# Performance work log

Measured on AMD Instinct MI355X. Metric: run time of the kernel, lower is better.

Reference implementation:

```python
import jax, jax.numpy as jnp
import numpy as np

N = 100000
DEG = 16
E = N * DEG
IN_F = 128
OUT_F = 64
ALPHA = 0.2  # LeakyReLU negative slope


def setup_inputs() -> dict:
    key = jax.random.key(0)
    k1, k2, k3, k4, k5, k6 = jax.random.split(key, 6)
    x = jax.random.normal(k1, (N, IN_F), dtype=jnp.float32)
    # src = repeat(arange(N), DEG) guarantees every node has outgoing edges
    # (original torch code divides by the out-edge score sum -> NaN otherwise).
    src = jnp.repeat(jnp.arange(N, dtype=jnp.int64), DEG)
    dst = jax.random.randint(k2, (E,), 0, N, dtype=jnp.int64)
    edges = jnp.stack([src, dst], axis=0)
    # Conv1d(in, out, k=1, bias=False) == linear with weight [out, in]
    w_seq = jax.random.normal(k3, (OUT_F, IN_F), dtype=jnp.float32) / np.sqrt(IN_F)
    # a_1, a_2: Conv1d(out, 1, k=1) with bias
    a1_w = jax.random.normal(k4, (OUT_F,), dtype=jnp.float32) / np.sqrt(OUT_F)
    a1_b = jnp.zeros((), dtype=jnp.float32)
    a2_w = jax.random.normal(k5, (OUT_F,), dtype=jnp.float32) / np.sqrt(OUT_F)
    a2_b = jnp.zeros((), dtype=jnp.float32)
    bias = jnp.zeros((OUT_F,), dtype=jnp.float32)
    return {"x": x, "edges": edges, "w_seq": w_seq, "a1_w": a1_w,
            "a1_b": a1_b, "a2_w": a2_w, "a2_b": a2_b, "bias": bias}


def reference(x, edges, w_seq, a1_w, a1_b, a2_w, a2_b, bias):
    src, dst = edges[0], edges[1]
    feat = x @ w_seq.T                       # [N, OUT_F]
    a1 = feat @ a1_w + a1_b                  # [N]
    a2 = feat @ a2_w + a2_b                  # [N]
    score = a1[src] + a2[dst]                # [E]
    score = jnp.exp(jax.nn.leaky_relu(score, ALPHA))
    score_sum = jax.ops.segment_sum(score, src, num_segments=N)  # [N]
    # sparse COO (score at (src,dst)) @ feat == segment_sum of score * feat[dst]
    msgs = score[:, None] * feat[dst]        # [E, OUT_F]
    agg = jax.ops.segment_sum(msgs, src, num_segments=N)         # [N, OUT_F]
    out = agg / score_sum[:, None] + bias
    return out
```

## Files before the change

kernel.cpp:

```cpp
#include <hip/hip_runtime.h>
#include <stdint.h>

#define N_NODES 100000
#define DEG 16
#define IN_F 128
#define OUT_F 64
#define ALPHA 0.2f

typedef __attribute__((ext_vector_type(8))) short short8;
typedef __attribute__((ext_vector_type(4))) float f32x4;
typedef __attribute__((ext_vector_type(4))) int i32x4;
typedef __attribute__((ext_vector_type(2))) unsigned int u32x2;

static __device__ __forceinline__ short f2bf(float f) {
    uint32_t u = __float_as_uint(f);
    u += 0x7FFFu + ((u >> 16) & 1u);
    return (short)(u >> 16);
}

__global__ __launch_bounds__(256) void w_conv_kernel(const float* __restrict__ w,
                                                     unsigned short* __restrict__ wb) {
    int idx = blockIdx.x * 256 + threadIdx.x;
    if (idx < OUT_F * IN_F) wb[idx] = (unsigned short)f2bf(w[idx]);
}

__global__ __launch_bounds__(256) void gat_feat_kernel(
    const float* __restrict__ x, const unsigned short* __restrict__ wb,
    const float* __restrict__ a1w, const float* __restrict__ a1bp,
    const float* __restrict__ a2w, const float* __restrict__ a2bp,
    unsigned short* __restrict__ featb, float* __restrict__ a1,
    float* __restrict__ a2)
{
    __shared__ __align__(16) unsigned short lds[4][32][64];
    const int wid  = threadIdx.x >> 6;
    const int lane = threadIdx.x & 63;
    const int r = lane & 15;
    const int g = lane >> 4;
    const int base = (blockIdx.x * 4 + wid) * 32;
    if (base >= N_NODES) return;

    short8 bfrag[4][4];
    #pragma unroll
    for (int ft = 0; ft < 4; ++ft)
        #pragma unroll
        for (int ks = 0; ks < 4; ++ks)
            bfrag[ft][ks] = *(const short8*)(wb + (ft * 16 + r) * IN_F + ks * 32 + g * 8);

    f32x4 acc[2][4];
    #pragma unroll
    for (int mt = 0; mt < 2; ++mt)
        #pragma unroll
        for (int ft = 0; ft < 4; ++ft) acc[mt][ft] = (f32x4){0.f, 0.f, 0.f, 0.f};

    #pragma unroll
    for (int mt = 0; mt < 2; ++mt) {
        const float* xrow = x + (size_t)(base + mt * 16 + r) * IN_F;
        #pragma unroll
        for (int ks = 0; ks < 4; ++ks) {
            const float* xp = xrow + ks * 32 + g * 8;
            f32x4 x0 = *(const f32x4*)(xp);
            f32x4 x1 = *(const f32x4*)(xp + 4);
            short8 af;
            af[0] = f2bf(x0[0]); af[1] = f2bf(x0[1]);
            af[2] = f2bf(x0[2]); af[3] = f2bf(x0[3]);
            af[4] = f2bf(x1[0]); af[5] = f2bf(x1[1]);
            af[6] = f2bf(x1[2]); af[7] = f2bf(x1[3]);
            #pragma unroll
            for (int ft = 0; ft < 4; ++ft)
                acc[mt][ft] = __builtin_amdgcn_mfma_f32_16x16x32_bf16(af, bfrag[ft][ks], acc[mt][ft], 0, 0, 0);
        }
    }

    float w1v[4], w2v[4];
    #pragma unroll
    for (int ft = 0; ft < 4; ++ft) { w1v[ft] = a1w[ft * 16 + r]; w2v[ft] = a2w[ft * 16 + r]; }
    float p1[2][4] = {{0.f,0.f,0.f,0.f},{0.f,0.f,0.f,0.f}};
    float p2[2][4] = {{0.f,0.f,0.f,0.f},{0.f,0.f,0.f,0.f}};
    #pragma unroll
    for (int mt = 0; mt < 2; ++mt)
        #pragma unroll
        for (int ft = 0; ft < 4; ++ft)
            #pragma unroll
            for (int reg = 0; reg < 4; ++reg) {
                p1[mt][reg] += acc[mt][ft][reg] * w1v[ft];
                p2[mt][reg] += acc[mt][ft][reg] * w2v[ft];
            }
    #pragma unroll
    for (int m = 1; m <= 8; m <<= 1)
        #pragma unroll
        for (int mt = 0; mt < 2; ++mt)
            #pragma unroll
            for (int reg = 0; reg < 4; ++reg) {
                p1[mt][reg] += __shfl_xor(p1[mt][reg], m, 64);
                p2[mt][reg] += __shfl_xor(p2[mt][reg], m, 64);
            }
    if (r == 0) {
        float b1 = a1bp[0], b2 = a2bp[0];
        #pragma unroll
        for (int mt = 0; mt < 2; ++mt)
            #pragma unroll
            for (int reg = 0; reg < 4; ++reg) {
                a1[base + mt * 16 + g * 4 + reg] = p1[mt][reg] + b1;
                a2[base + mt * 16 + g * 4 + reg] = p2[mt][reg] + b2;
            }
    }

    #pragma unroll
    for (int mt = 0; mt < 2; ++mt)
        #pragma unroll
        for (int ft = 0; ft < 4; ++ft)
            #pragma unroll
            for (int reg = 0; reg < 4; ++reg)
                lds[wid][mt * 16 + g * 4 + reg][ft * 16 + r] = (unsigned short)f2bf(acc[mt][ft][reg]);
    const char* lsrc = (const char*)(&lds[wid][0][0]);
    char* gdst = (char*)featb + (size_t)base * (OUT_F * 2);
    #pragma unroll
    for (int t = 0; t < 4; ++t) {
        i32x4 v = *(const i32x4*)(lsrc + t * 1024 + lane * 16);
        *(i32x4*)(gdst + t * 1024 + lane * 16) = v;
    }
}

__global__ __launch_bounds__(256) void gat_agg_kernel(
    const int* __restrict__ dst, const unsigned short* __restrict__ featb,
    const float* __restrict__ a1, const float* __restrict__ a2,
    const float* __restrict__ bias, float* __restrict__ out)
{
    const int wid  = threadIdx.x >> 6;
    const int lane = threadIdx.x & 63;
    const int q  = lane >> 4;
    const int e0 = lane & 15;
    const int i = (blockIdx.x * 4 + wid) * 4 + q;

    const int d = dst[i * DEG + e0];
    const float z = a1[i] + a2[d];
    const float s = __expf(z >= 0.f ? z : ALPHA * z);
    float ssum = s;
    #pragma unroll
    for (int m = 1; m <= 8; m <<= 1) ssum += __shfl_xor(ssum, m, 64);
    const float inv = 1.0f / ssum;

    float acc0 = 0.f, acc1 = 0.f, acc2 = 0.f, acc3 = 0.f;
    const int srcbase = lane & 48;
    #pragma unroll
    for (int e = 0; e < DEG; ++e) {
        const int   de = __shfl(d, srcbase + e, 64);
        const float se = __shfl(s, srcbase + e, 64);
        u32x2 u = *(const u32x2*)(featb + (size_t)(de * OUT_F + e0 * 4));
        acc0 += se * __uint_as_float(u[0] << 16);
        acc1 += se * __uint_as_float(u[0] & 0xffff0000u);
        acc2 += se * __uint_as_float(u[1] << 16);
        acc3 += se * __uint_as_float(u[1] & 0xffff0000u);
    }
    const f32x4 bv = *(const f32x4*)(bias + e0 * 4);
    f32x4 o;
    o[0] = acc0 * inv + bv[0];
    o[1] = acc1 * inv + bv[1];
    o[2] = acc2 * inv + bv[2];
    o[3] = acc3 * inv + bv[3];
    *(f32x4*)(out + (size_t)i * OUT_F + e0 * 4) = o;
}

extern "C" void kernel_launch(void* const* d_in, const int* in_sizes, int n_in,
                              void* d_out, int out_size, void* d_ws, size_t ws_size,
                              hipStream_t stream) {
    (void)in_sizes; (void)n_in; (void)out_size; (void)ws_size;
    const float* x    = (const float*)d_in[0];
    const int*   edges= (const int*)d_in[1];
    const float* w    = (const float*)d_in[2];
    const float* a1w  = (const float*)d_in[3];
    const float* a1b  = (const float*)d_in[4];
    const float* a2w  = (const float*)d_in[5];
    const float* a2b  = (const float*)d_in[6];
    const float* bias = (const float*)d_in[7];
    float* out = (float*)d_out;

    unsigned short* featb = (unsigned short*)d_ws;
    float* a1 = (float*)((char*)d_ws + (size_t)N_NODES * OUT_F * 2);
    float* a2 = a1 + N_NODES;
    unsigned short* wb = (unsigned short*)d_out;

    const int* dst = edges + (size_t)N_NODES * DEG;

    w_conv_kernel<<<dim3((OUT_F * IN_F + 255) / 256), dim3(256), 0, stream>>>(w, wb);
    gat_feat_kernel<<<dim3((N_NODES + 127) / 128), dim3(256), 0, stream>>>(
        x, wb, a1w, a1b, a2w, a2b, featb, a1, a2);
    gat_agg_kernel<<<dim3((N_NODES + 15) / 16), dim3(256), 0, stream>>>(
        dst, featb, a1, a2, bias, out);
}
```

Measured before the change: 58.10 us.

## Fold attention vectors into weights and batch gathers in aggregation

Precomputes v1 = W^T a1w and v2 = W^T a2w in the prep kernel, so a1/a2 are computed as fp32 dot products of x with these vectors during the feature pass. This replaces the post-MFMA projection and its 16-lane shuffle reduction. The aggregation kernel now issues its 16 neighbor gathers in two batches of 8 independent loads to raise memory-level parallelism, with the score shuffles hoisted. The bf16 weight fragments are now loaded per k-step instead of all up front, which lowers register pressure but adds extra loads, and the workspace layout gains v1/v2 and moves wb off the output buffer.

```diff
diff --git a/kernel.cpp b/kernel.cpp
--- a/kernel.cpp
+++ b/kernel.cpp
@@ -12,22 +12,34 @@
 typedef __attribute__((ext_vector_type(4))) int i32x4;
 typedef __attribute__((ext_vector_type(2))) unsigned int u32x2;
 
-static __device__ __forceinline__ short f2bf(float f) {
+static __device__ __forceinline__ unsigned short f2bf(float f) {
     uint32_t u = __float_as_uint(f);
     u += 0x7FFFu + ((u >> 16) & 1u);
-    return (short)(u >> 16);
-}
-
-__global__ __launch_bounds__(256) void w_conv_kernel(const float* __restrict__ w,
-                                                     unsigned short* __restrict__ wb) {
+    return (unsigned short)(u >> 16);
+}
+
+__global__ __launch_bounds__(256) void prep_kernel(
+    const float* __restrict__ w, const float* __restrict__ a1w,
+    const float* __restrict__ a2w, unsigned short* __restrict__ wb,
+    float* __restrict__ v1, float* __restrict__ v2)
+{
     int idx = blockIdx.x * 256 + threadIdx.x;
-    if (idx < OUT_F * IN_F) wb[idx] = (unsigned short)f2bf(w[idx]);
+    if (idx < OUT_F * IN_F) wb[idx] = f2bf(w[idx]);
+    if (blockIdx.x == 0) {
+        int t = threadIdx.x;
+        int k = t & (IN_F - 1);
+        const float* aw = (t < IN_F) ? a1w : a2w;
+        float acc = 0.f;
+        #pragma unroll
+        for (int f = 0; f < OUT_F; ++f) acc += w[f * IN_F + k] * aw[f];
+        if (t < IN_F) v1[k] = acc; else v2[k] = acc;
+    }
 }
 
 __global__ __launch_bounds__(256) void gat_feat_kernel(
     const float* __restrict__ x, const unsigned short* __restrict__ wb,
-    const float* __restrict__ a1w, const float* __restrict__ a1bp,
-    const float* __restrict__ a2w, const float* __restrict__ a2bp,
+    const float* __restrict__ v1, const float* __restrict__ v2,
+    const float* __restrict__ a1bp, const float* __restrict__ a2bp,
     unsigned short* __restrict__ featb, float* __restrict__ a1,
     float* __restrict__ a2)
 {
@@ -39,70 +51,58 @@
     const int base = (blockIdx.x * 4 + wid) * 32;
     if (base >= N_NODES) return;
 
-    short8 bfrag[4][4];
-    #pragma unroll
-    for (int ft = 0; ft < 4; ++ft)
-        #pragma unroll
-        for (int ks = 0; ks < 4; ++ks)
-            bfrag[ft][ks] = *(const short8*)(wb + (ft * 16 + r) * IN_F + ks * 32 + g * 8);
-
     f32x4 acc[2][4];
     #pragma unroll
     for (int mt = 0; mt < 2; ++mt)
         #pragma unroll
         for (int ft = 0; ft < 4; ++ft) acc[mt][ft] = (f32x4){0.f, 0.f, 0.f, 0.f};
-
-    #pragma unroll
-    for (int mt = 0; mt < 2; ++mt) {
-        const float* xrow = x + (size_t)(base + mt * 16 + r) * IN_F;
-        #pragma unroll
-        for (int ks = 0; ks < 4; ++ks) {
-            const float* xp = xrow + ks * 32 + g * 8;
+    float p1[2] = {0.f, 0.f}, p2[2] = {0.f, 0.f};
+
+    #pragma unroll
+    for (int ks = 0; ks < 4; ++ks) {
+        short8 bf[4];
+        #pragma unroll
+        for (int ft = 0; ft < 4; ++ft)
+            bf[ft] = *(const short8*)(wb + (ft * 16 + r) * IN_F + ks * 32 + g * 8);
+        const float* vp1 = v1 + ks * 32 + g * 8;
+        const float* vp2 = v2 + ks * 32 + g * 8;
+        f32x4 v10 = *(const f32x4*)(vp1),     v11 = *(const f32x4*)(vp1 + 4);
+        f32x4 v20 = *(const f32x4*)(vp2),     v21 = *(const f32x4*)(vp2 + 4);
+        #pragma unroll
+        for (int mt = 0; mt < 2; ++mt) {
+            const float* xp = x + (size_t)(base + mt * 16 + r) * IN_F + ks * 32 + g * 8;
             f32x4 x0 = *(const f32x4*)(xp);
             f32x4 x1 = *(const f32x4*)(xp + 4);
+            #pragma unroll
+            for (int j = 0; j < 4; ++j) {
+                p1[mt] += x0[j] * v10[j] + x1[j] * v11[j];
+                p2[mt] += x0[j] * v20[j] + x1[j] * v21[j];
+            }
             short8 af;
-            af[0] = f2bf(x0[0]); af[1] = f2bf(x0[1]);
-            af[2] = f2bf(x0[2]); af[3] = f2bf(x0[3]);
-            af[4] = f2bf(x1[0]); af[5] = f2bf(x1[1]);
-            af[6] = f2bf(x1[2]); af[7] = f2bf(x1[3]);
+            af[0] = (short)f2bf(x0[0]); af[1] = (short)f2bf(x0[1]);
+            af[2] = (short)f2bf(x0[2]); af[3] = (short)f2bf(x0[3]);
+            af[4] = (short)f2bf(x1[0]); af[5] = (short)f2bf(x1[1]);
+            af[6] = (short)f2bf(x1[2]); af[7] = (short)f2bf(x1[3]);
             #pragma unroll
             for (int ft = 0; ft < 4; ++ft)
-                acc[mt][ft] = __builtin_amdgcn_mfma_f32_16x16x32_bf16(af, bfrag[ft][ks], acc[mt][ft], 0, 0, 0);
+                acc[mt][ft] = __builtin_amdgcn_mfma_f32_16x16x32_bf16(af, bf[ft], acc[mt][ft], 0, 0, 0);
         }
     }
 
-    float w1v[4], w2v[4];
-    #pragma unroll
-    for (int ft = 0; ft < 4; ++ft) { w1v[ft] = a1w[ft * 16 + r]; w2v[ft] = a2w[ft * 16 + r]; }
-    float p1[2][4] = {{0.f,0.f,0.f,0.f},{0.f,0.f,0.f,0.f}};
-    float p2[2][4] = {{0.f,0.f,0.f,0.f},{0.f,0.f,0.f,0.f}};
-    #pragma unroll
-    for (int mt = 0; mt < 2; ++mt)
-        #pragma unroll
-        for (int ft = 0; ft < 4; ++ft)
-            #pragma unroll
-            for (int reg = 0; reg < 4; ++reg) {
-                p1[mt][reg] += acc[mt][ft][reg] * w1v[ft];
-                p2[mt][reg] += acc[mt][ft][reg] * w2v[ft];
-            }
-    #pragma unroll
-    for (int m = 1; m <= 8; m <<= 1)
-        #pragma unroll
-        for (int mt = 0; mt < 2; ++mt)
-            #pragma unroll
-            for (int reg = 0; reg < 4; ++reg) {
-                p1[mt][reg] += __shfl_xor(p1[mt][reg], m, 64);
-                p2[mt][reg] += __shfl_xor(p2[mt][reg], m, 64);
-            }
-    if (r == 0) {
+    #pragma unroll
+    for (int mt = 0; mt < 2; ++mt) {
+        p1[mt] += __shfl_xor(p1[mt], 16, 64);
+        p1[mt] += __shfl_xor(p1[mt], 32, 64);
+        p2[mt] += __shfl_xor(p2[mt], 16, 64);
+        p2[mt] += __shfl_xor(p2[mt], 32, 64);
+    }
+    if (lane < 16) {
         float b1 = a1bp[0], b2 = a2bp[0];
         #pragma unroll
-        for (int mt = 0; mt < 2; ++mt)
-            #pragma unroll
-            for (int reg = 0; reg < 4; ++reg) {
-                a1[base + mt * 16 + g * 4 + reg] = p1[mt][reg] + b1;
-                a2[base + mt * 16 + g * 4 + reg] = p2[mt][reg] + b2;
-            }
+        for (int mt = 0; mt < 2; ++mt) {
+            a1[base + mt * 16 + lane] = p1[mt] + b1;
+            a2[base + mt * 16 + lane] = p2[mt] + b2;
+        }
     }
 
     #pragma unroll
@@ -111,7 +111,7 @@
         for (int ft = 0; ft < 4; ++ft)
             #pragma unroll
             for (int reg = 0; reg < 4; ++reg)
-                lds[wid][mt * 16 + g * 4 + reg][ft * 16 + r] = (unsigned short)f2bf(acc[mt][ft][reg]);
+                lds[wid][mt * 16 + g * 4 + reg][ft * 16 + r] = f2bf(acc[mt][ft][reg]);
     const char* lsrc = (const char*)(&lds[wid][0][0]);
     char* gdst = (char*)featb + (size_t)base * (OUT_F * 2);
     #pragma unroll
@@ -131,27 +131,49 @@
     const int q  = lane >> 4;
     const int e0 = lane & 15;
     const int i = (blockIdx.x * 4 + wid) * 4 + q;
+    const int sb = lane & 48;
 
     const int d = dst[i * DEG + e0];
     const float z = a1[i] + a2[d];
-    const float s = __expf(z >= 0.f ? z : ALPHA * z);
-    float ssum = s;
-    #pragma unroll
-    for (int m = 1; m <= 8; m <<= 1) ssum += __shfl_xor(ssum, m, 64);
+    const float s = __expf(fmaxf(z, ALPHA * z));
+
+    float se[16];
+    float acc0 = 0.f, acc1 = 0.f, acc2 = 0.f, acc3 = 0.f;
+
+    int de[8];
+    #pragma unroll
+    for (int e = 0; e < 8; ++e) de[e] = __shfl(d, sb + e, 64);
+    u32x2 u[8];
+    #pragma unroll
+    for (int e = 0; e < 8; ++e)
+        u[e] = *(const u32x2*)(featb + ((size_t)de[e] * OUT_F + e0 * 4));
+    #pragma unroll
+    for (int e = 0; e < 16; ++e) se[e] = __shfl(s, sb + e, 64);
+    float ssum = 0.f;
+    #pragma unroll
+    for (int e = 0; e < 16; ++e) ssum += se[e];
+    #pragma unroll
+    for (int e = 0; e < 8; ++e) {
+        acc0 += se[e] * __uint_as_float(u[e][0] << 16);
+        acc1 += se[e] * __uint_as_float(u[e][0] & 0xffff0000u);
+        acc2 += se[e] * __uint_as_float(u[e][1] << 16);
+        acc3 += se[e] * __uint_as_float(u[e][1] & 0xffff0000u);
+    }
+
+    #pragma unroll
+    for (int e = 0; e < 8; ++e) de[e] = __shfl(d, sb + 8 + e, 64);
+    #pragma unroll
+    for (int e = 0; e < 8; ++e)
+        u[e] = *(const u32x2*)(featb + ((size_t)de[e] * OUT_F + e0 * 4));
+    #pragma unroll
+    for (int e = 0; e < 8; ++e) {
+        acc0 += se[8 + e] * __uint_as_float(u[e][0] << 16);
+        acc1 += se[8 + e] * __uint_as_float(u[e][0] & 0xffff0000u);
+        acc2 += se[8 + e] * __uint_as_float(u[e][1] << 16);
+        acc3 += se[8 + e] * __uint_as_float(u[e][1] & 0xffff0000u);
+    }
+
     const float inv = 1.0f / ssum;
-
-    float acc0 = 0.f, acc1 = 0.f, acc2 = 0.f, acc3 = 0.f;
-    const int srcbase = lane & 48;
-    #pragma unroll
-    for (int e = 0; e < DEG; ++e) {
-        const int   de = __shfl(d, srcbase + e, 64);
-        const float se = __shfl(s, srcbase + e, 64);
-        u32x2 u = *(const u32x2*)(featb + (size_t)(de * OUT_F + e0 * 4));
-        acc0 += se * __uint_as_float(u[0] << 16);
-        acc1 += se * __uint_as_float(u[0] & 0xffff0000u);
-        acc2 += se * __uint_as_float(u[1] << 16);
-        acc3 += se * __uint_as_float(u[1] & 0xffff0000u);
-    }
     const f32x4 bv = *(const f32x4*)(bias + e0 * 4);
     f32x4 o;
     o[0] = acc0 * inv + bv[0];
@@ -178,13 +200,16 @@
     unsigned short* featb = (unsigned short*)d_ws;
     float* a1 = (float*)((char*)d_ws + (size_t)N_NODES * OUT_F * 2);
     float* a2 = a1 + N_NODES;
-    unsigned short* wb = (unsigned short*)d_out;
+    float* v1 = a2 + N_NODES;
+    float* v2 = v1 + IN_F;
+    unsigned short* wb = (unsigned short*)(v2 + IN_F);
 
     const int* dst = edges + (size_t)N_NODES * DEG;
 
-    w_conv_kernel<<<dim3((OUT_F * IN_F + 255) / 256), dim3(256), 0, stream>>>(w, wb);
+    prep_kernel<<<dim3((OUT_F * IN_F + 255) / 256), dim3(256), 0, stream>>>(
+        w, a1w, a2w, wb, v1, v2);
     gat_feat_kernel<<<dim3((N_NODES + 127) / 128), dim3(256), 0, stream>>>(
-        x, wb, a1w, a1b, a2w, a2b, featb, a1, a2);
+        x, wb, v1, v2, a1b, a2b, featb, a1, a2);
     gat_agg_kernel<<<dim3((N_NODES + 15) / 16), dim3(256), 0, stream>>>(
         dst, featb, a1, a2, bias, out);
 }
```

New measurement: 57.83 us. No clear change (-0.5%).
